# Kernel tuning notes

Measured on AMD Instinct MI355X. Metric: run time of the kernel, lower is better.

## Reference

```python
import jax, jax.numpy as jnp
import numpy as np

B, T, D = 8, 4097, 512
H = 8
WIN = 64


def setup_inputs() -> dict:
    key = jax.random.key(0)
    k1, k2, k3 = jax.random.split(key, 3)
    x = jax.random.normal(k1, (B, T, D), dtype=jnp.float32)
    w_qkv = jax.random.normal(k2, (D, 3 * D), dtype=jnp.float32) * 0.02
    w_out = jax.random.normal(k3, (D, D), dtype=jnp.float32) * 0.02
    return {"x": x, "w_qkv": w_qkv, "w_out": w_out}


def reference(x, w_qkv, w_out):
    b, t, d_model = x.shape
    d = d_model // H
    scale = d ** (-0.5)
    nw = (t - 1) // WIN  # number of full windows over bbox tokens

    qkv = x @ w_qkv  # [B, T, 3D]
    q, k, v = jnp.split(qkv, 3, axis=-1)
    # [B, H, T, d]
    to_heads = lambda z: z.reshape(b, t, H, d).transpose(0, 2, 1, 3)
    q, k, v = to_heads(q), to_heads(k), to_heads(v)

    # global token (index 0) attends to ALL tokens
    q0 = q[:, :, :1]  # [B, H, 1, d]
    attn0 = jax.nn.softmax(jnp.einsum('bhqd,bhkd->bhqk', q0, k) * scale, axis=-1)
    out0 = jnp.einsum('bhqk,bhkd->bhqd', attn0, v)  # [B, H, 1, d]

    # bbox tokens: local attention within non-overlapping windows (no global token in keys)
    qw = q[:, :, 1:].reshape(b, H, nw, WIN, d)
    kw = k[:, :, 1:].reshape(b, H, nw, WIN, d)
    vw = v[:, :, 1:].reshape(b, H, nw, WIN, d)
    s = jnp.einsum('bhnqd,bhnkd->bhnqk', qw, kw) * scale
    attn = jax.nn.softmax(s, axis=-1)
    ow = jnp.einsum('bhnqk,bhnkd->bhnqd', attn, vw).reshape(b, H, t - 1, d)

    out = jnp.concatenate([out0, ow], axis=2)  # [B, H, T, d]
    out = out.transpose(0, 2, 1, 3).reshape(b, t, d_model)
    return out @ w_out
```

## Files before the change

### kernel.cpp

```cpp
#include <hip/hip_runtime.h>
#include <hip/hip_bf16.h>
#include <cstdint>
#include <cstddef>

using bf16 = __hip_bfloat16;
using short8 = __attribute__((ext_vector_type(8))) short;
using f32x4  = __attribute__((ext_vector_type(4))) float;

constexpr int Bc = 8;
constexpr int Tc = 4097;
constexpr int Dc = 512;
constexpr int Hc = 8;
constexpr int Mrows = Bc * Tc;
constexpr int Mpad2 = 33024;
constexpr int NCh = 65;

__device__ __forceinline__ float bf2f(unsigned short u) {
    union { unsigned int i; float f; } v;
    v.i = ((unsigned int)u) << 16;
    return v.f;
}

__device__ __forceinline__ unsigned short f2b(float f) {
    union { float f; unsigned int i; } u; u.f = f;
    unsigned int r = u.i + 0x7FFFu + ((u.i >> 16) & 1u);
    return (unsigned short)(r >> 16);
}

__device__ __forceinline__ void gload_lds16(const void* g, void* l) {
    __builtin_amdgcn_global_load_lds(
        (const __attribute__((address_space(1))) void*)g,
        (__attribute__((address_space(3))) void*)l, 16, 0, 0);
}

__global__ __launch_bounds__(256)
void k_cvt_x(const float* __restrict__ x, bf16* __restrict__ xb)
{
    size_t i8 = ((size_t)blockIdx.x * 256 + threadIdx.x) * 8;
    if (i8 >= (size_t)Mpad2 * 512) return;
    union { short s[8]; short8 v; } o;
    if (i8 < (size_t)Mrows * 512) {
        float4 v0 = *(const float4*)(x + i8);
        float4 v1 = *(const float4*)(x + i8 + 4);
        o.s[0] = (short)f2b(v0.x); o.s[1] = (short)f2b(v0.y);
        o.s[2] = (short)f2b(v0.z); o.s[3] = (short)f2b(v0.w);
        o.s[4] = (short)f2b(v1.x); o.s[5] = (short)f2b(v1.y);
        o.s[6] = (short)f2b(v1.z); o.s[7] = (short)f2b(v1.w);
    } else {
        o.v = short8{0,0,0,0,0,0,0,0};
    }
    *(short8*)((short*)xb + i8) = o.v;
}

__global__ __launch_bounds__(256)
void k_cvt_wT(const float* __restrict__ w, bf16* __restrict__ wT, int K, int N)
{
    __shared__ float t[32][33];
    int bn = blockIdx.x * 32, bk = blockIdx.y * 32;
    int tx = threadIdx.x & 31, ty = threadIdx.x >> 5;
    #pragma unroll
    for (int j = 0; j < 4; ++j)
        t[ty + j * 8][tx] = w[(size_t)(bk + ty + j * 8) * N + bn + tx];
    __syncthreads();
    #pragma unroll
    for (int j = 0; j < 4; ++j)
        wT[(size_t)(bn + ty + j * 8) * K + bk + tx] =
            __float2bfloat16(t[tx][ty + j * 8]);
}

template <typename OutT, int NT>
__global__ __launch_bounds__(256)
void k_gemm_dbuf(const bf16* __restrict__ A, const bf16* __restrict__ Bt,
                 OutT* __restrict__ C, int Mlim)
{
    constexpr int N = NT * 128;
    __shared__ short lds[32768];

    const int tid = threadIdx.x;
    const int lane = tid & 63, wave = tid >> 6;
    const int lo = lane & 15, g = lane >> 4;
    const int wr = wave >> 1, wc = wave & 1;

    const int nwg = 257 * NT;
    const int orig = blockIdx.x;
    const int qq = nwg >> 3, rr = nwg & 7;
    const int xc = orig & 7, o8 = orig >> 3;
    const int swz = (xc < rr ? xc * (qq + 1) : rr * (qq + 1) + (xc - rr) * qq) + o8;
    const int bm = (swz / NT) * 128, bn = (swz % NT) * 128;

    const bf16* aSrc[4]; const bf16* bSrc[4];
    int dstOff[4];
    #pragma unroll
    for (int i = 0; i < 4; ++i) {
        int d = i * 256 + tid;
        int row = d >> 3, c = d & 7;
        int ck = (c - row) & 7;
        aSrc[i] = A  + (size_t)(bm + row) * 512 + ck * 8;
        bSrc[i] = Bt + (size_t)(bn + row) * 512 + ck * 8;
        dstOff[i] = d * 8;
    }

    auto STAGE = [&](int kt) {
        const int bb = (kt & 1) * 16384;
        #pragma unroll
        for (int i = 0; i < 4; ++i)
            gload_lds16(aSrc[i] + kt * 64, lds + bb + dstOff[i]);
        #pragma unroll
        for (int i = 0; i < 4; ++i)
            gload_lds16(bSrc[i] + kt * 64, lds + bb + 8192 + dstOff[i]);
    };

    const int colk[2] = { (g + (lo & 7)) & 7, (g + 4 + (lo & 7)) & 7 };
    const int arow0 = wr * 64 + lo;
    const int brow0 = wc * 64 + lo;

    f32x4 acc[4][4] = {};

    STAGE(0);
    STAGE(1);
    asm volatile("s_waitcnt vmcnt(8)" ::: "memory");
    __builtin_amdgcn_s_barrier();

    for (int t = 0; t < 8; ++t) {
        const short* bufA = lds + (t & 1) * 16384;
        const short* bufB = bufA + 8192;

        #pragma unroll
        for (int ks = 0; ks < 2; ++ks) {
            const int col = colk[ks];
            short8 af[4], bfr[4];
            #pragma unroll
            for (int mi = 0; mi < 4; ++mi)
                af[mi] = *(const short8*)(bufA + (arow0 + mi * 16) * 64 + col * 8);
            #pragma unroll
            for (int ni = 0; ni < 4; ++ni)
                bfr[ni] = *(const short8*)(bufB + (brow0 + ni * 16) * 64 + col * 8);
            __builtin_amdgcn_s_setprio(1);
            #pragma unroll
            for (int mi = 0; mi < 4; ++mi)
                #pragma unroll
                for (int ni = 0; ni < 4; ++ni)
                    acc[mi][ni] = __builtin_amdgcn_mfma_f32_16x16x32_bf16(
                        bfr[ni], af[mi], acc[mi][ni], 0, 0, 0);
            __builtin_amdgcn_s_setprio(0);
        }

        asm volatile("s_waitcnt lgkmcnt(0)" ::: "memory");
        __builtin_amdgcn_s_barrier();
        if (t < 6) {
            STAGE(t + 2);
            asm volatile("s_waitcnt vmcnt(8)" ::: "memory");
            __builtin_amdgcn_s_barrier();
        } else if (t == 6) {
            asm volatile("s_waitcnt vmcnt(0)" ::: "memory");
            __builtin_amdgcn_s_barrier();
        }
    }

    #pragma unroll
    for (int mi = 0; mi < 4; ++mi) {
        int m = bm + wr * 64 + mi * 16 + lo;
        if (m < Mlim) {
            #pragma unroll
            for (int ni = 0; ni < 4; ++ni) {
                int n = bn + wc * 64 + ni * 16 + g * 4;
                if constexpr (sizeof(OutT) == 2) {
                    ushort4 o = { f2b(acc[mi][ni][0]), f2b(acc[mi][ni][1]),
                                  f2b(acc[mi][ni][2]), f2b(acc[mi][ni][3]) };
                    *(ushort4*)((bf16*)C + (size_t)m * N + n) = o;
                } else {
                    float4 o = { acc[mi][ni][0], acc[mi][ni][1],
                                 acc[mi][ni][2], acc[mi][ni][3] };
                    *(float4*)((float*)C + (size_t)m * N + n) = o;
                }
            }
        }
    }
}

__global__ __launch_bounds__(256)
void k_attn_win(const bf16* __restrict__ qkv, bf16* __restrict__ aout)
{
    __shared__ __attribute__((aligned(16))) unsigned short pS[64 * 64];
    __shared__ __attribute__((aligned(16))) unsigned short vT[64 * 64];

    const int n = blockIdx.x, h = blockIdx.y, b = blockIdx.z;
    const int tid = threadIdx.x;
    const int wave = tid >> 6, lane = tid & 63;
    const int lo = lane & 15, g = lane >> 4;

    const bf16* base = qkv + ((size_t)b * Tc + 1 + (size_t)n * 64) * 1536 + h * 64;
    const bf16* kbase = base + 512;
    const bf16* vbase = base + 1024;

    {
        const int key = tid & 63;
        const int d0 = (tid >> 6) * 16;
        const bf16* vp = vbase + (size_t)key * 1536 + d0;
        ushort4 u[4];
        #pragma unroll
        for (int q = 0; q < 4; ++q) u[q] = *(const ushort4*)(vp + q * 4);
        const unsigned short vals[16] = {
            u[0].x, u[0].y, u[0].z, u[0].w, u[1].x, u[1].y, u[1].z, u[1].w,
            u[2].x, u[2].y, u[2].z, u[2].w, u[3].x, u[3].y, u[3].z, u[3].w };
        #pragma unroll
        for (int j = 0; j < 16; ++j) {
            int d = d0 + j;
            int byteoff = d * 128 + ((key * 2) ^ ((d & 7) << 4));
            *(unsigned short*)((char*)vT + byteoff) = vals[j];
        }
    }

    short8 qf[2];
    {
        const bf16* qp = base + (size_t)(wave * 16 + lo) * 1536 + g * 8;
        qf[0] = *(const short8*)(qp);
        qf[1] = *(const short8*)(qp + 32);
    }

    f32x4 sacc[4] = {};
    #pragma unroll
    for (int ni = 0; ni < 4; ++ni) {
        const bf16* kp = kbase + (size_t)(ni * 16 + lo) * 1536 + g * 8;
        short8 k0 = *(const short8*)(kp);
        short8 k1 = *(const short8*)(kp + 32);
        sacc[ni] = __builtin_amdgcn_mfma_f32_16x16x32_bf16(qf[0], k0, sacc[ni], 0, 0, 0);
        sacc[ni] = __builtin_amdgcn_mfma_f32_16x16x32_bf16(qf[1], k1, sacc[ni], 0, 0, 0);
    }

    __syncthreads();

    float pv[4][4];
    float inv[4];
    #pragma unroll
    for (int r = 0; r < 4; ++r) {
        float m = fmaxf(fmaxf(sacc[0][r], sacc[1][r]),
                        fmaxf(sacc[2][r], sacc[3][r])) * 0.125f;
        m = fmaxf(m, __shfl_xor(m, 1));
        m = fmaxf(m, __shfl_xor(m, 2));
        m = fmaxf(m, __shfl_xor(m, 4));
        m = fmaxf(m, __shfl_xor(m, 8));
        float s = 0.f;
        #pragma unroll
        for (int ni = 0; ni < 4; ++ni) {
            float e = __expf(sacc[ni][r] * 0.125f - m);
            pv[ni][r] = e;
            s += e;
        }
        s += __shfl_xor(s, 1);
        s += __shfl_xor(s, 2);
        s += __shfl_xor(s, 4);
        s += __shfl_xor(s, 8);
        inv[r] = 1.f / s;
    }

    #pragma unroll
    for (int ni = 0; ni < 4; ++ni) {
        #pragma unroll
        for (int r = 0; r < 4; ++r) {
            int qrow = wave * 16 + g * 4 + r;
            int col = ni * 16 + lo;
            int byteoff = qrow * 128 + ((col * 2) ^ ((qrow & 7) << 4));
            *(unsigned short*)((char*)pS + byteoff) = f2b(pv[ni][r]);
        }
    }
    __syncthreads();

    f32x4 oacc[4] = {};
    #pragma unroll
    for (int s = 0; s < 2; ++s) {
        int arow2 = wave * 16 + lo;
        int abyte = arow2 * 128 + (((s * 32 + g * 8) * 2) ^ ((arow2 & 7) << 4));
        short8 pa = *(const short8*)((const char*)pS + abyte);
        #pragma unroll
        for (int nd = 0; nd < 4; ++nd) {
            int d = nd * 16 + lo;
            int bbyte = d * 128 + (((s * 32 + g * 8) * 2) ^ ((d & 7) << 4));
            short8 vb = *(const short8*)((const char*)vT + bbyte);
            oacc[nd] = __builtin_amdgcn_mfma_f32_16x16x32_bf16(pa, vb, oacc[nd], 0, 0, 0);
        }
    }

    #pragma unroll
    for (int nd = 0; nd < 4; ++nd) {
        #pragma unroll
        for (int r = 0; r < 4; ++r) {
            int t = 1 + n * 64 + wave * 16 + g * 4 + r;
            aout[((size_t)b * Tc + t) * Dc + h * 64 + nd * 16 + lo] =
                __float2bfloat16(oacc[nd][r] * inv[r]);
        }
    }
}

__global__ __launch_bounds__(64)
void k_tok0_part(const bf16* __restrict__ qkv, float* __restrict__ part)
{
    const int c = blockIdx.x, h = blockIdx.y, b = blockIdx.z;
    const int lane = threadIdx.x;
    __shared__ float q0s[64];
    __shared__ float vS[64][65];
    __shared__ float pSm[64];

    q0s[lane] = bf2f(*(const unsigned short*)
        (qkv + (size_t)b * Tc * 1536 + h * 64 + lane));
    __syncthreads();

    const int t = c * 64 + lane;
    const bool valid = t < Tc;
    float logit = -1e30f;
    if (valid) {
        const bf16* kp = qkv + ((size_t)b * Tc + t) * 1536 + 512 + h * 64;
        float l = 0.f;
        #pragma unroll
        for (int d4 = 0; d4 < 16; ++d4) {
            ushort4 ku = ((const ushort4*)kp)[d4];
            l = fmaf(q0s[d4 * 4 + 0], bf2f(ku.x), l);
            l = fmaf(q0s[d4 * 4 + 1], bf2f(ku.y), l);
            l = fmaf(q0s[d4 * 4 + 2], bf2f(ku.z), l);
            l = fmaf(q0s[d4 * 4 + 3], bf2f(ku.w), l);
        }
        logit = l * 0.125f;
        const bf16* vp = kp + 512;
        #pragma unroll
        for (int d4 = 0; d4 < 16; ++d4) {
            ushort4 vu = ((const ushort4*)vp)[d4];
            vS[lane][d4 * 4 + 0] = bf2f(vu.x);
            vS[lane][d4 * 4 + 1] = bf2f(vu.y);
            vS[lane][d4 * 4 + 2] = bf2f(vu.z);
            vS[lane][d4 * 4 + 3] = bf2f(vu.w);
        }
    } else {
        #pragma unroll
        for (int d = 0; d < 64; ++d) vS[lane][d] = 0.f;
    }

    float m = logit;
    #pragma unroll
    for (int off = 1; off < 64; off <<= 1) m = fmaxf(m, __shfl_xor(m, off));
    float p = valid ? __expf(logit - m) : 0.f;
    float s = p;
    #pragma unroll
    for (int off = 1; off < 64; off <<= 1) s += __shfl_xor(s, off);
    pSm[lane] = p;
    __syncthreads();

    float o = 0.f;
    #pragma unroll
    for (int i = 0; i < 64; ++i) o = fmaf(pSm[i], vS[i][lane], o);

    float* pout = part + ((size_t)(b * Hc + h) * NCh + c) * 66;
    pout[lane] = o;
    if (lane == 0) { pout[64] = m; pout[65] = s; }
}

__global__ __launch_bounds__(64)
void k_tok0_reduce(const float* __restrict__ part, bf16* __restrict__ aout)
{
    const int h = blockIdx.x, b = blockIdx.y;
    const int lane = threadIdx.x;
    const float* base = part + (size_t)(b * Hc + h) * NCh * 66;

    float M = -1e30f;
    for (int c = 0; c < NCh; ++c) M = fmaxf(M, base[c * 66 + 64]);

    float S = 0.f, o = 0.f;
    for (int c = 0; c < NCh; ++c) {
        const float* pp = base + c * 66;
        float w = __expf(pp[64] - M);
        S += pp[65] * w;
        o = fmaf(pp[lane], w, o);
    }
    aout[(size_t)b * Tc * Dc + h * 64 + lane] = __float2bfloat16(o / S);
}

extern "C" void kernel_launch(void* const* d_in, const int* in_sizes, int n_in,
                              void* d_out, int out_size, void* d_ws, size_t ws_size,
                              hipStream_t stream)
{
    const float* x     = (const float*)d_in[0];
    const float* w_qkv = (const float*)d_in[1];
    const float* w_out = (const float*)d_in[2];
    float* out = (float*)d_out;

    bf16* qkv = (bf16*)d_ws;
    bf16* xa  = qkv + (size_t)Mrows * 1536;
    bf16* wqT = xa  + (size_t)Mpad2 * 512;
    bf16* woT = wqT + (size_t)1536 * 512;
    float* part = (float*)wqT;

    {
        int nblk = (int)(((size_t)Mpad2 * 512 / 8 + 255) / 256);
        k_cvt_x<<<nblk, 256, 0, stream>>>(x, xa);
    }
    k_cvt_wT<<<dim3(48, 16), 256, 0, stream>>>(w_qkv, wqT, 512, 1536);
    k_cvt_wT<<<dim3(16, 16), 256, 0, stream>>>(w_out, woT, 512, 512);

    k_gemm_dbuf<bf16, 12><<<257 * 12, 256, 0, stream>>>(xa, wqT, qkv, Mrows);

    k_attn_win<<<dim3(64, Hc, Bc), 256, 0, stream>>>(qkv, xa);
    k_tok0_part<<<dim3(NCh, Hc, Bc), dim3(64), 0, stream>>>(qkv, part);
    k_tok0_reduce<<<dim3(Hc, Bc), dim3(64), 0, stream>>>(part, xa);

    k_gemm_dbuf<float, 4><<<257 * 4, 256, 0, stream>>>(xa, woT, out, Mrows);
}
```

Before: 183.7 us.

## Replace double-buffered GEMM with triple-buffered BK=32 pipeline and larger QKV tiles

Rewrites the bf16 MFMA GEMM into a templated kernel that uses a three-stage LDS ring with K-step 32. The next tile's global-to-LDS load is issued before the current tile's compute, and there is one barrier per step instead of two. The QKV projection now runs 512-thread workgroups on 256x128 tiles (129x12 blocks) to improve operand reuse. The output projection keeps 128x128 tiles under the new pipeline. The risks are more loop iterations with a smaller K per step, a different LDS swizzle, and possible occupancy or register pressure from the larger tiles.

```diff
diff --git a/kernel.cpp b/kernel.cpp
--- a/kernel.cpp
+++ b/kernel.cpp
@@ -31,6 +31,13 @@
     __builtin_amdgcn_global_load_lds(
         (const __attribute__((address_space(1))) void*)g,
         (__attribute__((address_space(3))) void*)l, 16, 0, 0);
+}
+
+template <int N> __device__ __forceinline__ void waitvm() {
+    if constexpr (N == 0) asm volatile("s_waitcnt vmcnt(0)" ::: "memory");
+    else if constexpr (N == 3) asm volatile("s_waitcnt vmcnt(3)" ::: "memory");
+    else if constexpr (N == 4) asm volatile("s_waitcnt vmcnt(4)" ::: "memory");
+    else static_assert(N == 0, "unsupported vmcnt");
 }
 
 __global__ __launch_bounds__(256)
@@ -68,93 +75,95 @@
             __float2bfloat16(t[tx][ty + j * 8]);
 }
 
-template <typename OutT, int NT>
-__global__ __launch_bounds__(256)
-void k_gemm_dbuf(const bf16* __restrict__ A, const bf16* __restrict__ Bt,
+template <typename OutT, int WR, int WC, int NT, int MINW>
+__global__ __launch_bounds__(WR * WC * 64, MINW)
+void k_gemm_pipe(const bf16* __restrict__ A, const bf16* __restrict__ Bt,
                  OutT* __restrict__ C, int Mlim)
 {
-    constexpr int N = NT * 128;
-    __shared__ short lds[32768];
-
-    const int tid = threadIdx.x;
+    constexpr int T  = WR * WC * 64;
+    constexpr int BM = WR * 64;
+    constexpr int BN = WC * 64;
+    constexpr int N  = NT * BN;
+    constexpr int SZ = (BM + BN) * 32;
+    constexpr int LOADS = ((BM + BN) * 4) / T;
+    constexpr int NK = 16;
+    __shared__ short lds[3 * SZ];
+
+    const int tid  = threadIdx.x;
     const int lane = tid & 63, wave = tid >> 6;
     const int lo = lane & 15, g = lane >> 4;
-    const int wr = wave >> 1, wc = wave & 1;
-
-    const int nwg = 257 * NT;
+    const int wr = wave / WC, wc = wave % WC;
+
+    const int nwg = 129 * (BM / 256 == 0 ? 0 : 0) + gridDim.x;
     const int orig = blockIdx.x;
     const int qq = nwg >> 3, rr = nwg & 7;
     const int xc = orig & 7, o8 = orig >> 3;
     const int swz = (xc < rr ? xc * (qq + 1) : rr * (qq + 1) + (xc - rr) * qq) + o8;
-    const int bm = (swz / NT) * 128, bn = (swz % NT) * 128;
-
-    const bf16* aSrc[4]; const bf16* bSrc[4];
-    int dstOff[4];
+    const int bm = (swz / NT) * BM, bn = (swz % NT) * BN;
+
+    const bf16* src[LOADS];
+    int dst[LOADS];
+    #pragma unroll
+    for (int i = 0; i < LOADS; ++i) {
+        int d = i * T + tid;
+        if (d < BM * 4) {
+            int row = d >> 2, c = d & 3, ck = (c - row) & 3;
+            src[i] = A + (size_t)(bm + row) * 512 + ck * 8;
+            dst[i] = d * 8;
+        } else {
+            int dd = d - BM * 4;
+            int row = dd >> 2, c = dd & 3, ck = (c - row) & 3;
+            src[i] = Bt + (size_t)(bn + row) * 512 + ck * 8;
+            dst[i] = BM * 32 + dd * 8;
+        }
+    }
+
+    auto STAGE = [&](int kt, int bb) {
+        #pragma unroll
+        for (int i = 0; i < LOADS; ++i)
+            gload_lds16(src[i] + kt * 32, lds + bb + dst[i]);
+    };
+
+    int aoff[4], boff[4];
     #pragma unroll
     for (int i = 0; i < 4; ++i) {
-        int d = i * 256 + tid;
-        int row = d >> 3, c = d & 7;
-        int ck = (c - row) & 7;
-        aSrc[i] = A  + (size_t)(bm + row) * 512 + ck * 8;
-        bSrc[i] = Bt + (size_t)(bn + row) * 512 + ck * 8;
-        dstOff[i] = d * 8;
-    }
-
-    auto STAGE = [&](int kt) {
-        const int bb = (kt & 1) * 16384;
-        #pragma unroll
-        for (int i = 0; i < 4; ++i)
-            gload_lds16(aSrc[i] + kt * 64, lds + bb + dstOff[i]);
-        #pragma unroll
-        for (int i = 0; i < 4; ++i)
-            gload_lds16(bSrc[i] + kt * 64, lds + bb + 8192 + dstOff[i]);
-    };
-
-    const int colk[2] = { (g + (lo & 7)) & 7, (g + 4 + (lo & 7)) & 7 };
-    const int arow0 = wr * 64 + lo;
-    const int brow0 = wc * 64 + lo;
+        int ar = wr * 64 + i * 16 + lo;
+        aoff[i] = ar * 32 + ((g + ar) & 3) * 8;
+        int br = wc * 64 + i * 16 + lo;
+        boff[i] = BM * 32 + br * 32 + ((g + br) & 3) * 8;
+    }
 
     f32x4 acc[4][4] = {};
 
-    STAGE(0);
-    STAGE(1);
-    asm volatile("s_waitcnt vmcnt(8)" ::: "memory");
-    __builtin_amdgcn_s_barrier();
-
-    for (int t = 0; t < 8; ++t) {
-        const short* bufA = lds + (t & 1) * 16384;
-        const short* bufB = bufA + 8192;
-
-        #pragma unroll
-        for (int ks = 0; ks < 2; ++ks) {
-            const int col = colk[ks];
-            short8 af[4], bfr[4];
-            #pragma unroll
-            for (int mi = 0; mi < 4; ++mi)
-                af[mi] = *(const short8*)(bufA + (arow0 + mi * 16) * 64 + col * 8);
+    STAGE(0, 0);
+    STAGE(1, SZ);
+    waitvm<LOADS>();
+    asm volatile("s_barrier" ::: "memory");
+
+    for (int t = 0; t < NK; ++t) {
+        const int rb = (t % 3) * SZ;
+        if (t < NK - 2) STAGE(t + 2, ((t + 2) % 3) * SZ);
+
+        const short* bufp = lds + rb;
+        short8 af[4], bfr[4];
+        #pragma unroll
+        for (int i = 0; i < 4; ++i) af[i] = *(const short8*)(bufp + aoff[i]);
+        #pragma unroll
+        for (int i = 0; i < 4; ++i) bfr[i] = *(const short8*)(bufp + boff[i]);
+
+        __builtin_amdgcn_s_setprio(1);
+        #pragma unroll
+        for (int mi = 0; mi < 4; ++mi)
             #pragma unroll
             for (int ni = 0; ni < 4; ++ni)
-                bfr[ni] = *(const short8*)(bufB + (brow0 + ni * 16) * 64 + col * 8);
-            __builtin_amdgcn_s_setprio(1);
-            #pragma unroll
-            for (int mi = 0; mi < 4; ++mi)
-                #pragma unroll
-                for (int ni = 0; ni < 4; ++ni)
-                    acc[mi][ni] = __builtin_amdgcn_mfma_f32_16x16x32_bf16(
-                        bfr[ni], af[mi], acc[mi][ni], 0, 0, 0);
-            __builtin_amdgcn_s_setprio(0);
-        }
+                acc[mi][ni] = __builtin_amdgcn_mfma_f32_16x16x32_bf16(
+                    bfr[ni], af[mi], acc[mi][ni], 0, 0, 0);
+        __builtin_amdgcn_s_setprio(0);
 
         asm volatile("s_waitcnt lgkmcnt(0)" ::: "memory");
-        __builtin_amdgcn_s_barrier();
-        if (t < 6) {
-            STAGE(t + 2);
-            asm volatile("s_waitcnt vmcnt(8)" ::: "memory");
-            __builtin_amdgcn_s_barrier();
-        } else if (t == 6) {
-            asm volatile("s_waitcnt vmcnt(0)" ::: "memory");
-            __builtin_amdgcn_s_barrier();
-        }
+        if (t < NK - 2)       waitvm<LOADS>();
+        else if (t == NK - 2) waitvm<0>();
+        if (t < NK - 1) asm volatile("s_barrier" ::: "memory");
     }
 
     #pragma unroll
@@ -395,11 +404,13 @@
     k_cvt_wT<<<dim3(48, 16), 256, 0, stream>>>(w_qkv, wqT, 512, 1536);
     k_cvt_wT<<<dim3(16, 16), 256, 0, stream>>>(w_out, woT, 512, 512);
 
-    k_gemm_dbuf<bf16, 12><<<257 * 12, 256, 0, stream>>>(xa, wqT, qkv, Mrows);
+    k_gemm_pipe<bf16, 4, 2, 12, 4><<<129 * 12, 512, 0, stream>>>(
+        xa, wqT, qkv, Mrows);
 
     k_attn_win<<<dim3(64, Hc, Bc), 256, 0, stream>>>(qkv, xa);
     k_tok0_part<<<dim3(NCh, Hc, Bc), dim3(64), 0, stream>>>(qkv, part);
     k_tok0_reduce<<<dim3(Hc, Bc), dim3(64), 0, stream>>>(part, xa);
 
-    k_gemm_dbuf<float, 4><<<257 * 4, 256, 0, stream>>>(xa, woT, out, Mrows);
-}
+    k_gemm_pipe<float, 2, 2, 4, 3><<<257 * 4, 256, 0, stream>>>(
+        xa, woT, out, Mrows);
+}
```

After: 196.5 us. 1.07x slower.

## Fuse global-token partial attention into windowed attention kernel

Applied to the files above, without the earlier changes.

The separate global-token partial kernel goes away. Each windowed-attention block now also computes the token-0 query's logits against its window's 64 keys and forms the partial weighted V sum from the V tile already held in LDS. It then writes max, sum and partial output for a later reduction. The reduce kernel now handles token 0's own key and value directly. This avoids re-reading K/V from global memory and removes a kernel launch, at the cost of extra work, LDS and a sync in the window kernel.

```diff
diff --git a/kernel.cpp b/kernel.cpp
--- a/kernel.cpp
+++ b/kernel.cpp
@@ -13,7 +13,7 @@
 constexpr int Hc = 8;
 constexpr int Mrows = Bc * Tc;
 constexpr int Mpad2 = 33024;
-constexpr int NCh = 65;
+constexpr int NW = 64;
 
 __device__ __forceinline__ float bf2f(unsigned short u) {
     union { unsigned int i; float f; } v;
@@ -179,10 +179,14 @@
 }
 
 __global__ __launch_bounds__(256)
-void k_attn_win(const bf16* __restrict__ qkv, bf16* __restrict__ aout)
+void k_attn_win(const bf16* __restrict__ qkv, bf16* __restrict__ aout,
+                float* __restrict__ part)
 {
     __shared__ __attribute__((aligned(16))) unsigned short pS[64 * 64];
     __shared__ __attribute__((aligned(16))) unsigned short vT[64 * 64];
+    __shared__ float q0s[64];
+    __shared__ float pTok[64];
+    __shared__ float oPart[4][64];
 
     const int n = blockIdx.x, h = blockIdx.y, b = blockIdx.z;
     const int tid = threadIdx.x;
@@ -210,6 +214,10 @@
             *(unsigned short*)((char*)vT + byteoff) = vals[j];
         }
     }
+
+    if (tid < 64)
+        q0s[tid] = bf2f(*(const unsigned short*)
+            (qkv + (size_t)b * Tc * 1536 + h * 64 + tid));
 
     short8 qf[2];
     {
@@ -229,6 +237,29 @@
     }
 
     __syncthreads();
+
+    float m_w = 0.f, s_w = 0.f;
+    if (wave == 0) {
+        const bf16* kp = kbase + (size_t)lane * 1536;
+        float l = 0.f;
+        #pragma unroll
+        for (int d8 = 0; d8 < 8; ++d8) {
+            short8 kv = *(const short8*)(kp + d8 * 8);
+            #pragma unroll
+            for (int e = 0; e < 8; ++e)
+                l = fmaf(q0s[d8 * 8 + e], bf2f((unsigned short)kv[e]), l);
+        }
+        l *= 0.125f;
+        float mm = l;
+        #pragma unroll
+        for (int off = 1; off < 64; off <<= 1) mm = fmaxf(mm, __shfl_xor(mm, off));
+        float p = __expf(l - mm);
+        float ss = p;
+        #pragma unroll
+        for (int off = 1; off < 64; off <<= 1) ss += __shfl_xor(ss, off);
+        pTok[lane] = p;
+        m_w = mm; s_w = ss;
+    }
 
     float pv[4][4];
     float inv[4];
@@ -281,6 +312,20 @@
         }
     }
 
+    {
+        const int d = tid & 63, qq = tid >> 6;
+        float po = 0.f;
+        #pragma unroll
+        for (int j16 = 0; j16 < 16; ++j16) {
+            int j = qq * 16 + j16;
+            int byteoff = d * 128 + ((j * 2) ^ ((d & 7) << 4));
+            po = fmaf(pTok[j],
+                      bf2f(*(const unsigned short*)((const char*)vT + byteoff)),
+                      po);
+        }
+        oPart[qq][d] = po;
+    }
+
     #pragma unroll
     for (int nd = 0; nd < 4; ++nd) {
         #pragma unroll
@@ -290,86 +335,48 @@
                 __float2bfloat16(oacc[nd][r] * inv[r]);
         }
     }
+
+    __syncthreads();
+
+    if (tid < 64) {
+        float o0 = oPart[0][tid] + oPart[1][tid] + oPart[2][tid] + oPart[3][tid];
+        float* pout = part + ((size_t)(b * Hc + h) * NW + n) * 66;
+        pout[tid] = o0;
+        if (tid == 0) { pout[64] = m_w; pout[65] = s_w; }
+    }
 }
 
 __global__ __launch_bounds__(64)
-void k_tok0_part(const bf16* __restrict__ qkv, float* __restrict__ part)
-{
-    const int c = blockIdx.x, h = blockIdx.y, b = blockIdx.z;
-    const int lane = threadIdx.x;
-    __shared__ float q0s[64];
-    __shared__ float vS[64][65];
-    __shared__ float pSm[64];
-
-    q0s[lane] = bf2f(*(const unsigned short*)
-        (qkv + (size_t)b * Tc * 1536 + h * 64 + lane));
-    __syncthreads();
-
-    const int t = c * 64 + lane;
-    const bool valid = t < Tc;
-    float logit = -1e30f;
-    if (valid) {
-        const bf16* kp = qkv + ((size_t)b * Tc + t) * 1536 + 512 + h * 64;
-        float l = 0.f;
-        #pragma unroll
-        for (int d4 = 0; d4 < 16; ++d4) {
-            ushort4 ku = ((const ushort4*)kp)[d4];
-            l = fmaf(q0s[d4 * 4 + 0], bf2f(ku.x), l);
-            l = fmaf(q0s[d4 * 4 + 1], bf2f(ku.y), l);
-            l = fmaf(q0s[d4 * 4 + 2], bf2f(ku.z), l);
-            l = fmaf(q0s[d4 * 4 + 3], bf2f(ku.w), l);
-        }
-        logit = l * 0.125f;
-        const bf16* vp = kp + 512;
-        #pragma unroll
-        for (int d4 = 0; d4 < 16; ++d4) {
-            ushort4 vu = ((const ushort4*)vp)[d4];
-            vS[lane][d4 * 4 + 0] = bf2f(vu.x);
-            vS[lane][d4 * 4 + 1] = bf2f(vu.y);
-            vS[lane][d4 * 4 + 2] = bf2f(vu.z);
-            vS[lane][d4 * 4 + 3] = bf2f(vu.w);
-        }
-    } else {
-        #pragma unroll
-        for (int d = 0; d < 64; ++d) vS[lane][d] = 0.f;
-    }
-
-    float m = logit;
-    #pragma unroll
-    for (int off = 1; off < 64; off <<= 1) m = fmaxf(m, __shfl_xor(m, off));
-    float p = valid ? __expf(logit - m) : 0.f;
-    float s = p;
-    #pragma unroll
-    for (int off = 1; off < 64; off <<= 1) s += __shfl_xor(s, off);
-    pSm[lane] = p;
-    __syncthreads();
-
-    float o = 0.f;
-    #pragma unroll
-    for (int i = 0; i < 64; ++i) o = fmaf(pSm[i], vS[i][lane], o);
-
-    float* pout = part + ((size_t)(b * Hc + h) * NCh + c) * 66;
-    pout[lane] = o;
-    if (lane == 0) { pout[64] = m; pout[65] = s; }
-}
-
-__global__ __launch_bounds__(64)
-void k_tok0_reduce(const float* __restrict__ part, bf16* __restrict__ aout)
+void k_tok0_reduce(const float* __restrict__ part, const bf16* __restrict__ qkv,
+                   bf16* __restrict__ aout)
 {
     const int h = blockIdx.x, b = blockIdx.y;
     const int lane = threadIdx.x;
-    const float* base = part + (size_t)(b * Hc + h) * NCh * 66;
-
-    float M = -1e30f;
-    for (int c = 0; c < NCh; ++c) M = fmaxf(M, base[c * 66 + 64]);
+    const float* basep = part + (size_t)(b * Hc + h) * NW * 66;
+    const bf16* qrow = qkv + (size_t)b * Tc * 1536 + h * 64;
+
+    float l0 = bf2f(*(const unsigned short*)(qrow + lane)) *
+               bf2f(*(const unsigned short*)(qrow + 512 + lane));
+    #pragma unroll
+    for (int off = 1; off < 64; off <<= 1) l0 += __shfl_xor(l0, off);
+    l0 *= 0.125f;
+
+    float M = basep[lane * 66 + 64];
+    #pragma unroll
+    for (int off = 1; off < 64; off <<= 1) M = fmaxf(M, __shfl_xor(M, off));
+    M = fmaxf(M, l0);
 
     float S = 0.f, o = 0.f;
-    for (int c = 0; c < NCh; ++c) {
-        const float* pp = base + c * 66;
+    for (int c = 0; c < NW; ++c) {
+        const float* pp = basep + c * 66;
         float w = __expf(pp[64] - M);
         S += pp[65] * w;
         o = fmaf(pp[lane], w, o);
     }
+    float p0 = __expf(l0 - M);
+    S += p0;
+    o = fmaf(p0, bf2f(*(const unsigned short*)(qrow + 1024 + lane)), o);
+
     aout[(size_t)b * Tc * Dc + h * 64 + lane] = __float2bfloat16(o / S);
 }
 
@@ -397,9 +404,8 @@
 
     k_gemm_dbuf<bf16, 12><<<257 * 12, 256, 0, stream>>>(xa, wqT, qkv, Mrows);
 
-    k_attn_win<<<dim3(64, Hc, Bc), 256, 0, stream>>>(qkv, xa);
-    k_tok0_part<<<dim3(NCh, Hc, Bc), dim3(64), 0, stream>>>(qkv, part);
-    k_tok0_reduce<<<dim3(Hc, Bc), dim3(64), 0, stream>>>(part, xa);
+    k_attn_win<<<dim3(64, Hc, Bc), 256, 0, stream>>>(qkv, xa, part);
+    k_tok0_reduce<<<dim3(Hc, Bc), dim3(64), 0, stream>>>(part, qkv, xa);
 
     k_gemm_dbuf<float, 4><<<257 * 4, 256, 0, stream>>>(xa, woT, out, Mrows);
 }
```

Result: faster. 167.0 us (-9.1%).
